# Performance work log

Hardware: AMD Instinct MI355X
Metric: run time of the kernel (lower is better)

## Reference

```python
import jax, jax.numpy as jnp
import numpy as np
from jax import lax


def _attention_conv(x, Wq, bq, Wk, bk, Wv, bv, head_w, p):
    # x: [B,C,H,W]; Wq/Wk/Wv: [heads, D, D] (torch Linear weight, out x in); b*: [heads, D]
    B, C, H, W = x.shape
    pad_h = (p * (1 + H // p) - H) % p
    pad_w = (p * (1 + W // p) - W) % p
    xp = jnp.pad(x, ((0, 0), (0, 0), (p + pad_h, p), (p + pad_w, p)), mode='reflect')
    num_h = (H + pad_h) // p
    num_w = (W + pad_w) // p
    # view padded image as a grid of (num_h+2) x (num_w+2) patches of size p x p
    g = xp.reshape(B, C, num_h + 2, p, num_w + 2, p)
    # 9-patch neighborhood per window (equivalent to unfold with window=3p, stride=p)
    nb = jnp.stack([g[:, :, di:di + num_h, :, dj:dj + num_w, :]
                    for di in range(3) for dj in range(3)], axis=2)  # [B,C,9,num_h,p,num_w,p]
    tokens = nb.transpose(0, 3, 5, 2, 1, 4, 6).reshape(B * num_h * num_w, 9, C * p * p)
    D = C * p * p
    q = jnp.einsum('npd,hed->nhpe', tokens, Wq) + bq[None, :, None, :]
    k = jnp.einsum('npd,hed->nhpe', tokens, Wk) + bk[None, :, None, :]
    v = jnp.einsum('npd,hed->nhpe', tokens, Wv) + bv[None, :, None, :]
    # core patch (index 4 = center of 3x3) attends to all 9 patches
    score = jnp.einsum('nhe,nhpe->nhp', q[:, :, 4, :], k) / jnp.sqrt(jnp.float32(D))
    attn = jax.nn.softmax(score, axis=-1)               # [N,heads,9]
    out = jnp.einsum('nhp,nhpe->nhe', attn, v)          # [N,heads,D]
    mixed = jnp.einsum('h,nhe->ne', head_w[0], out)     # head-weight mixing -> [N,D]
    out = mixed.reshape(B, num_h, num_w, C, p, p).transpose(0, 3, 1, 4, 2, 5)
    out = out.reshape(B, C, num_h * p, num_w * p)
    return out[:, :, pad_h:, pad_w:]


def _dehaze(x, p3, p6, p9, conv0_w, conv0_b):
    b, c, h, w = x.shape
    avg = jnp.mean((1.0 - x).reshape(b, c, -1), axis=-1, keepdims=True)  # [b,c,1]
    xg1 = jax.nn.softmax(avg, axis=-1)[..., None]                        # softmax over size-1 dim -> ones
    xg = jnp.max((x * xg1).reshape(b, 1, -1), axis=-1, keepdims=True)[..., None]  # [b,1,1,1]
    x3 = _attention_conv(x, *p3, 1)
    x6 = _attention_conv(x3, *p6, 2)
    x9 = _attention_conv(x6, *p9, 3)
    cat = jnp.concatenate([x9, x6, x3], axis=1)
    x0 = jax.nn.relu(lax.conv_general_dilated(cat, conv0_w, (1, 1), [(2, 2), (2, 2)])
                     + conv0_b[None, :, None, None])
    return jax.nn.relu(x * x0 + (xg - x0))


def setup_inputs() -> dict:
    key = jax.random.key(0)
    ks = jax.random.split(key, 12)
    inp = {'x': jax.random.uniform(ks[0], (2, 3, 384, 384), jnp.float32)}
    specs = [('3', 6, 3), ('6', 4, 12), ('9', 2, 27)]  # (stage, num_heads, D=C*p*p)
    i = 1
    for name, h, d in specs:
        for proj in ('q', 'k', 'v'):
            inp['w%s_%s' % (name, proj)] = jax.random.normal(ks[i], (h, d, d), jnp.float32) * 0.02
            inp['b%s_%s' % (name, proj)] = jnp.zeros((h, d), jnp.float32)
            i += 1
        inp['hw%s' % name] = jnp.ones((1, h), jnp.float32) / h
    inp['conv0_w'] = jax.random.normal(ks[10], (3, 9, 5, 5), jnp.float32) * 0.02
    inp['conv0_b'] = jnp.zeros((3,), jnp.float32)
    return inp


def reference(x, w3_q, b3_q, w3_k, b3_k, w3_v, b3_v, hw3,
              w6_q, b6_q, w6_k, b6_k, w6_v, b6_v, hw6,
              w9_q, b9_q, w9_k, b9_k, w9_v, b9_v, hw9,
              conv0_w, conv0_b):
    p3 = (w3_q, b3_q, w3_k, b3_k, w3_v, b3_v, hw3)
    p6 = (w6_q, b6_q, w6_k, b6_k, w6_v, b6_v, hw6)
    p9 = (w9_q, b9_q, w9_k, b9_k, w9_v, b9_v, hw9)
    return _dehaze(x, p3, p6, p9, conv0_w, conv0_b)
```

## Files before the change

### kernel.cpp

```cpp
#include <hip/hip_runtime.h>

#define HH 384
#define HWPX (HH*HH)

#define WOFF3 16
#define HS3   40
#define WOFF6 256
#define HS6   328
#define WOFF9 1568
#define HS9   1600
#define CATOFF 8192
#define P9BOFF (CATOFF + 2*9*HWPX)
#define WS_NEED ((size_t)(P9BOFF + 2*3*HWPX) * 4)

__device__ __forceinline__ float4 fma4s(float4 a, float4 w, float t) {
    a.x += w.x * t; a.y += w.y * t; a.z += w.z * t; a.w += w.w * t; return a;
}
__device__ __forceinline__ float dot4(float4 a, float4 b) {
    return a.x * b.x + a.y * b.y + a.z * b.z + a.w * b.w;
}

__global__ __launch_bounds__(256) void pre_xg(
    const float* __restrict__ w3q, const float* __restrict__ b3q,
    const float* __restrict__ w3k, const float* __restrict__ b3k,
    const float* __restrict__ w3v, const float* __restrict__ b3v, const float* __restrict__ hw3,
    const float* __restrict__ w6q, const float* __restrict__ b6q,
    const float* __restrict__ w6k, const float* __restrict__ b6k,
    const float* __restrict__ w6v, const float* __restrict__ b6v, const float* __restrict__ hw6,
    const float* __restrict__ w9q, const float* __restrict__ b9q,
    const float* __restrict__ w9k, const float* __restrict__ b9k,
    const float* __restrict__ w9v, const float* __restrict__ b9v, const float* __restrict__ hw9,
    const float* __restrict__ x, float* __restrict__ ws)
{
    __shared__ float sm[4];
    const int blk = blockIdx.x;
    const int tid = threadIdx.x;

    if (blk < 12) {
        int stage = blk < 6 ? 0 : (blk < 10 ? 1 : 2);
        int h = blk - (stage == 0 ? 0 : (stage == 1 ? 6 : 10));
        const float* WQ[3] = {w3q, w6q, w9q};
        const float* BQ[3] = {b3q, b6q, b9q};
        const float* WK[3] = {w3k, w6k, w9k};
        const float* BK[3] = {b3k, b6k, b9k};
        const float* WV_[3] = {w3v, w6v, w9v};
        const float* BV[3] = {b3v, b6v, b9v};
        const float* HWp[3] = {hw3, hw6, hw9};
        const int Ds[3] = {3, 12, 27};
        const int DPs[3] = {4, 12, 28};
        const int WOFFs[3] = {WOFF3, WOFF6, WOFF9};
        const int HSs[3] = {HS3, HS6, HS9};

        const int D = Ds[stage], DP = DPs[stage];
        const float* wq = WQ[stage] + h * D * D;
        const float* bq = BQ[stage] + h * D;
        const float* wk = WK[stage] + h * D * D;
        const float* bk = BK[stage] + h * D;
        const float* wv = WV_[stage] + h * D * D;
        const float* bv = BV[stage] + h * D;
        const float hwv = HWp[stage][h];
        float* base = ws + WOFFs[stage] + h * HSs[stage];
        const float scale = rsqrtf((float)D);

        for (int i = tid; i < D * DP; i += 256) {
            int a = i / DP, b = i % DP;
            float m = 0.f;
            if (b < D) for (int e = 0; e < D; ++e) m += wk[e * D + b] * wq[e * D + a];
            base[i] = scale * m;
            float wvv = 0.f;
            if (b < D) wvv = hwv * wv[a * D + b];
            base[D * DP + i] = wvv;
        }
        for (int i = tid; i < DP; i += 256) {
            float cv = 0.f, uv = 0.f;
            if (i < D) for (int e = 0; e < D; ++e) {
                cv += bq[e] * wk[e * D + i];
                uv += wq[e * D + i] * bk[e];
            }
            base[2 * D * DP + i] = scale * cv;
            base[2 * D * DP + DP + i] = scale * uv;
            base[2 * D * DP + 2 * DP + i] = (i < D) ? hwv * bv[i] : 0.f;
        }
        if (tid == 0) {
            float s = 0.f;
            for (int e = 0; e < D; ++e) s += bq[e] * bk[e];
            base[2 * D * DP + 3 * DP] = scale * s;
        }
    } else {
        int i2 = blk - 12;
        int b = i2 / 144, chunk = i2 % 144;
        const float4* xb = (const float4*)(x + (size_t)b * 3 * HWPX + chunk * 3072);
        float m = 0.f;
        for (int j = tid; j < 768; j += 256) {
            float4 v = xb[j];
            m = fmaxf(m, fmaxf(fmaxf(v.x, v.y), fmaxf(v.z, v.w)));
        }
        for (int off = 32; off; off >>= 1)
            m = fmaxf(m, __shfl_down(m, off));
        if ((tid & 63) == 0) sm[tid >> 6] = m;
        __syncthreads();
        if (tid == 0) {
            float mm = fmaxf(fmaxf(sm[0], sm[1]), fmaxf(sm[2], sm[3]));
            atomicMax((int*)&ws[b], __float_as_int(mm));
        }
    }
}

template <int P, int HEADS, int HSPLIT>
__global__ __launch_bounds__(256) void attn_cell(
    const float* __restrict__ in, long in_bstride,
    float* __restrict__ outA, long outA_bstride,
    float* __restrict__ outB, long outB_bstride,
    const float* __restrict__ wsw)
{
    constexpr int C = 3, D = C * P * P, DP = (D + 3) & ~3, NREG = DP / 4;
    constexpr int HS = 2 * D * DP + 3 * DP + 4;
    constexpr int HPT = HEADS / HSPLIT;
    __shared__ __align__(16) float scell[324 * DP];
    __shared__ __align__(16) float sw[HPT * HS];

    const int tid = threadIdx.x;
    const int z = blockIdx.z;
    const int b = z & 1;
    const int hs = z >> 1;
    const int BWY = blockIdx.y * 16, BWX = blockIdx.x * 16;

    const float* inb = in + (size_t)b * in_bstride;
    constexpr int XW = 18 * P;
    constexpr int TOT = 3 * P * 18 * XW;
    for (int i = tid; i < TOT; i += 256) {
        int c = i / (P * 18 * XW);
        int rem = i % (P * 18 * XW);
        int r = rem / (18 * XW);
        int rem2 = rem % (18 * XW);
        int cy = rem2 / XW, xx = rem2 % XW;
        int y = (BWY + cy) * P + r - P; y = y < 0 ? -y : (y >= HH ? 2 * HH - 2 - y : y);
        int x = BWX * P + xx - P;       x = x < 0 ? -x : (x >= HH ? 2 * HH - 2 - x : x);
        int cx = xx / P, s = xx % P;
        scell[(cy * 18 + cx) * DP + (c * P + r) * P + s] = inb[c * HWPX + y * HH + x];
    }
    if constexpr (DP > D) {
        for (int j = tid; j < 324; j += 256) scell[j * DP + D] = 0.f;
    }
    const float* wsrc = wsw + (size_t)hs * HPT * HS;
    for (int i = tid; i < HPT * HS; i += 256) sw[i] = wsrc[i];
    __syncthreads();

    const int wx = tid & 15, wy = tid >> 4;

    float t4[DP];
    {
        const float4* T4p = (const float4*)&scell[((wy + 1) * 18 + wx + 1) * DP];
#pragma unroll
        for (int k = 0; k < NREG; ++k) {
            float4 v = T4p[k];
            t4[4 * k] = v.x; t4[4 * k + 1] = v.y; t4[4 * k + 2] = v.z; t4[4 * k + 3] = v.w;
        }
    }
    float mixed[D];
#pragma unroll
    for (int e = 0; e < D; ++e) mixed[e] = 0.f;

#pragma unroll 1
    for (int hh = 0; hh < HPT; ++hh) {
        const float* hb = sw + hh * HS;
        const float* ccb = hb + 2 * D * DP;
        float4 qk[NREG];
        {
            const float4* cp = (const float4*)ccb;
#pragma unroll
            for (int k = 0; k < NREG; ++k) qk[k] = cp[k];
        }
        float su = ccb[3 * DP];
#pragma unroll
        for (int a = 0; a < D; ++a) {
            const float t = t4[a];
            su += ccb[DP + a] * t;
            const float4* Mr = (const float4*)(hb + a * DP);
#pragma unroll
            for (int k = 0; k < NREG; ++k) qk[k] = fma4s(qk[k], Mr[k], t);
        }
        float denom = 0.f;
        float4 wt[NREG];
#pragma unroll
        for (int k = 0; k < NREG; ++k) wt[k] = make_float4(0.f, 0.f, 0.f, 0.f);
#pragma unroll
        for (int di = 0; di < 3; ++di)
#pragma unroll
            for (int dj = 0; dj < 3; ++dj) {
                const float4* cp = (const float4*)&scell[((wy + di) * 18 + wx + dj) * DP];
                float4 cv[NREG];
#pragma unroll
                for (int k = 0; k < NREG; ++k) cv[k] = cp[k];
                float s = su;
#pragma unroll
                for (int k = 0; k < NREG; ++k) s += dot4(qk[k], cv[k]);
                const float e = __expf(s);
                denom += e;
#pragma unroll
                for (int k = 0; k < NREG; ++k) wt[k] = fma4s(wt[k], cv[k], e);
            }
        const float winv = 1.f / denom;
#pragma unroll
        for (int k = 0; k < NREG; ++k) {
            wt[k].x *= winv; wt[k].y *= winv; wt[k].z *= winv; wt[k].w *= winv;
        }
        const float* WVb = hb + D * DP;
#pragma unroll
        for (int e = 0; e < D; ++e) {
            const float4* Wr = (const float4*)(WVb + e * DP);
            float o = ccb[2 * DP + e];
#pragma unroll
            for (int k = 0; k < NREG; ++k) o += dot4(Wr[k], wt[k]);
            mixed[e] += o;
        }
    }

    float* outp = (hs == 0) ? (outA + (size_t)b * outA_bstride)
                            : (outB + (size_t)b * outB_bstride);
#pragma unroll
    for (int c = 0; c < C; ++c)
#pragma unroll
        for (int r = 0; r < P; ++r)
#pragma unroll
            for (int s = 0; s < P; ++s)
                outp[c * HWPX + ((BWY + wy) * P + r) * HH + (BWX + wx) * P + s] =
                    mixed[(c * P + r) * P + s];
}

__global__ __launch_bounds__(128) void conv_final(
    const float* __restrict__ cat, const float* __restrict__ p9b, int addp9,
    const float* __restrict__ w, const float* __restrict__ bias,
    const float* __restrict__ x, const float* __restrict__ xg,
    float* __restrict__ out)
{
    __shared__ float tile[9][20][40];
    const int tid = threadIdx.x;
    const int b = blockIdx.z;
    const int bx = blockIdx.x * 32, by = blockIdx.y * 16;
    const float* catb = cat + (size_t)b * 9 * HWPX;
    const float* p9bb = p9b + (size_t)b * 3 * HWPX;

    for (int i = tid; i < 9 * 20 * 10; i += 128) {
        int ci = i / 200;
        int rem = i % 200;
        int row = rem / 10, c4 = rem % 10;
        int y = by + row - 2, xx = bx - 4 + 4 * c4;
        float4 v = {0.f, 0.f, 0.f, 0.f};
        if (y >= 0 && y < HH && xx >= 0 && xx <= HH - 4) {
            v = *(const float4*)&catb[ci * HWPX + y * HH + xx];
            if (addp9 && ci < 3) {
                float4 u = *(const float4*)&p9bb[ci * HWPX + y * HH + xx];
                v.x += u.x; v.y += u.y; v.z += u.z; v.w += u.w;
            }
        }
        *(float4*)&tile[ci][row][4 * c4] = v;
    }
    __syncthreads();

    const int tx = tid & 7, ty = tid >> 3;
    float acc0[4], acc1[4], acc2[4];
    const float b0 = bias[0], b1 = bias[1], b2 = bias[2];
#pragma unroll
    for (int j = 0; j < 4; ++j) { acc0[j] = b0; acc1[j] = b1; acc2[j] = b2; }

#pragma unroll
    for (int ky = 0; ky < 5; ++ky) {
#pragma unroll 1
        for (int ci = 0; ci < 9; ++ci) {
            const float4 ra = *(const float4*)&tile[ci][ty + ky][4 * tx];
            const float4 rb = *(const float4*)&tile[ci][ty + ky][4 * tx + 4];
            const float4 rc = *(const float4*)&tile[ci][ty + ky][4 * tx + 8];
            const float r[12] = {ra.x, ra.y, ra.z, ra.w, rb.x, rb.y, rb.z, rb.w,
                                 rc.x, rc.y, rc.z, rc.w};
            const float* __restrict__ w0 = w + (0 * 9 + ci) * 25 + ky * 5;
            const float* __restrict__ w1 = w + (1 * 9 + ci) * 25 + ky * 5;
            const float* __restrict__ w2 = w + (2 * 9 + ci) * 25 + ky * 5;
#pragma unroll
            for (int j = 0; j < 4; ++j)
#pragma unroll
                for (int kx = 0; kx < 5; ++kx) {
                    const float t = r[j + kx + 2];
                    acc0[j] += t * w0[kx];
                    acc1[j] += t * w1[kx];
                    acc2[j] += t * w2[kx];
                }
        }
    }

    const int yb = by + ty, xb = bx + 4 * tx;
    const float xgv = xg[b];
    float* accs[3] = {acc0, acc1, acc2};
#pragma unroll
    for (int co = 0; co < 3; ++co) {
        const float4 xv = *(const float4*)&x[((size_t)(b * 3 + co)) * HWPX + yb * HH + xb];
        const float* a = accs[co];
        float4 ov;
        float x0;
        x0 = fmaxf(a[0], 0.f); ov.x = fmaxf(xv.x * x0 + xgv - x0, 0.f);
        x0 = fmaxf(a[1], 0.f); ov.y = fmaxf(xv.y * x0 + xgv - x0, 0.f);
        x0 = fmaxf(a[2], 0.f); ov.z = fmaxf(xv.z * x0 + xgv - x0, 0.f);
        x0 = fmaxf(a[3], 0.f); ov.w = fmaxf(xv.w * x0 + xgv - x0, 0.f);
        *(float4*)&out[((size_t)(b * 3 + co)) * HWPX + yb * HH + xb] = ov;
    }
}

extern "C" void kernel_launch(void* const* d_in, const int* in_sizes, int n_in,
                              void* d_out, int out_size, void* d_ws, size_t ws_size,
                              hipStream_t stream) {
    const float* x   = (const float*)d_in[0];
    const float* w3q = (const float*)d_in[1];
    const float* b3q = (const float*)d_in[2];
    const float* w3k = (const float*)d_in[3];
    const float* b3k = (const float*)d_in[4];
    const float* w3v = (const float*)d_in[5];
    const float* b3v = (const float*)d_in[6];
    const float* hw3 = (const float*)d_in[7];
    const float* w6q = (const float*)d_in[8];
    const float* b6q = (const float*)d_in[9];
    const float* w6k = (const float*)d_in[10];
    const float* b6k = (const float*)d_in[11];
    const float* w6v = (const float*)d_in[12];
    const float* b6v = (const float*)d_in[13];
    const float* hw6 = (const float*)d_in[14];
    const float* w9q = (const float*)d_in[15];
    const float* b9q = (const float*)d_in[16];
    const float* w9k = (const float*)d_in[17];
    const float* b9k = (const float*)d_in[18];
    const float* w9v = (const float*)d_in[19];
    const float* b9v = (const float*)d_in[20];
    const float* hw9 = (const float*)d_in[21];
    const float* c0w = (const float*)d_in[22];
    const float* c0b = (const float*)d_in[23];

    float* out = (float*)d_out;
    float* ws  = (float*)d_ws;
    float* cat = ws + CATOFF;
    float* p9b = ws + P9BOFF;
    const bool split9 = ws_size >= WS_NEED;

    pre_xg<<<300, 256, 0, stream>>>(
        w3q, b3q, w3k, b3k, w3v, b3v, hw3,
        w6q, b6q, w6k, b6k, w6v, b6v, hw6,
        w9q, b9q, w9k, b9k, w9v, b9v, hw9, x, ws);

    attn_cell<1, 6, 1><<<dim3(24, 24, 2), 256, 0, stream>>>(
        x, 3 * HWPX, cat + 6 * HWPX, 9 * HWPX, cat + 6 * HWPX, 9 * HWPX, ws + WOFF3);
    attn_cell<2, 4, 1><<<dim3(12, 12, 2), 256, 0, stream>>>(
        cat + 6 * HWPX, 9 * HWPX, cat + 3 * HWPX, 9 * HWPX, cat + 3 * HWPX, 9 * HWPX, ws + WOFF6);
    if (split9)
        attn_cell<3, 2, 2><<<dim3(8, 8, 4), 256, 0, stream>>>(
            cat + 3 * HWPX, 9 * HWPX, cat, 9 * HWPX, p9b, 3 * HWPX, ws + WOFF9);
    else
        attn_cell<3, 2, 1><<<dim3(8, 8, 2), 256, 0, stream>>>(
            cat + 3 * HWPX, 9 * HWPX, cat, 9 * HWPX, cat, 9 * HWPX, ws + WOFF9);

    conv_final<<<dim3(12, 24, 2), 128, 0, stream>>>(
        cat, p9b, split9 ? 1 : 0, c0w, c0b, x, ws, out);
}
```

Measured before the change: 216.5 us.

## Fuse all three attention stages and final conv into one tiled megakernel

Replaces the three per-stage attention kernels and the final conv kernel with a single kernel. Each block loads a haloed input tile into LDS and computes the p=1, p=2 and p=3 stages with recomputed halos. Reflect-padding borders are fixed up in shared memory, and the 5x5 conv plus output epilogue run in place. This removes the global round trips of the intermediate concat buffers and three launches. In exchange it recomputes halo regions, leaves only 192 blocks to occupy the GPU, and runs the stage-9 pass on just 234 of 512 threads. An unused stub kernel 'mega' is also left in.

```diff
diff --git a/kernel.cpp b/kernel.cpp
--- a/kernel.cpp
+++ b/kernel.cpp
@@ -9,15 +9,19 @@
 #define HS6   328
 #define WOFF9 1568
 #define HS9   1600
-#define CATOFF 8192
-#define P9BOFF (CATOFF + 2*9*HWPX)
-#define WS_NEED ((size_t)(P9BOFF + 2*3*HWPX) * 4)
-
+
+__device__ __forceinline__ int rx(int g) {
+    g = g < 0 ? -g : g;
+    return g >= HH ? 2 * HH - 2 - g : g;
+}
 __device__ __forceinline__ float4 fma4s(float4 a, float4 w, float t) {
     a.x += w.x * t; a.y += w.y * t; a.z += w.z * t; a.w += w.w * t; return a;
 }
 __device__ __forceinline__ float dot4(float4 a, float4 b) {
     return a.x * b.x + a.y * b.y + a.z * b.z + a.w * b.w;
+}
+__device__ __forceinline__ float f4c(const float4& v, int j) {
+    return j == 0 ? v.x : (j == 1 ? v.y : (j == 2 ? v.z : v.w));
 }
 
 __global__ __launch_bounds__(256) void pre_xg(
@@ -106,202 +110,357 @@
     }
 }
 
-template <int P, int HEADS, int HSPLIT>
-__global__ __launch_bounds__(256) void attn_cell(
-    const float* __restrict__ in, long in_bstride,
-    float* __restrict__ outA, long outA_bstride,
-    float* __restrict__ outB, long outB_bstride,
-    const float* __restrict__ wsw)
-{
-    constexpr int C = 3, D = C * P * P, DP = (D + 3) & ~3, NREG = DP / 4;
-    constexpr int HS = 2 * D * DP + 3 * DP + 4;
-    constexpr int HPT = HEADS / HSPLIT;
-    __shared__ __align__(16) float scell[324 * DP];
-    __shared__ __align__(16) float sw[HPT * HS];
-
-    const int tid = threadIdx.x;
-    const int z = blockIdx.z;
-    const int b = z & 1;
-    const int hs = z >> 1;
-    const int BWY = blockIdx.y * 16, BWX = blockIdx.x * 16;
-
-    const float* inb = in + (size_t)b * in_bstride;
-    constexpr int XW = 18 * P;
-    constexpr int TOT = 3 * P * 18 * XW;
-    for (int i = tid; i < TOT; i += 256) {
-        int c = i / (P * 18 * XW);
-        int rem = i % (P * 18 * XW);
-        int r = rem / (18 * XW);
-        int rem2 = rem % (18 * XW);
-        int cy = rem2 / XW, xx = rem2 % XW;
-        int y = (BWY + cy) * P + r - P; y = y < 0 ? -y : (y >= HH ? 2 * HH - 2 - y : y);
-        int x = BWX * P + xx - P;       x = x < 0 ? -x : (x >= HH ? 2 * HH - 2 - x : x);
-        int cx = xx / P, s = xx % P;
-        scell[(cy * 18 + cx) * DP + (c * P + r) * P + s] = inb[c * HWPX + y * HH + x];
-    }
-    if constexpr (DP > D) {
-        for (int j = tid; j < 324; j += 256) scell[j * DP + D] = 0.f;
-    }
-    const float* wsrc = wsw + (size_t)hs * HPT * HS;
-    for (int i = tid; i < HPT * HS; i += 256) sw[i] = wsrc[i];
-    __syncthreads();
-
-    const int wx = tid & 15, wy = tid >> 4;
-
-    float t4[DP];
-    {
-        const float4* T4p = (const float4*)&scell[((wy + 1) * 18 + wx + 1) * DP];
-#pragma unroll
-        for (int k = 0; k < NREG; ++k) {
-            float4 v = T4p[k];
-            t4[4 * k] = v.x; t4[4 * k + 1] = v.y; t4[4 * k + 2] = v.z; t4[4 * k + 3] = v.w;
-        }
-    }
-    float mixed[D];
-#pragma unroll
-    for (int e = 0; e < D; ++e) mixed[e] = 0.f;
-
-#pragma unroll 1
-    for (int hh = 0; hh < HPT; ++hh) {
-        const float* hb = sw + hh * HS;
-        const float* ccb = hb + 2 * D * DP;
-        float4 qk[NREG];
-        {
-            const float4* cp = (const float4*)ccb;
-#pragma unroll
-            for (int k = 0; k < NREG; ++k) qk[k] = cp[k];
-        }
-        float su = ccb[3 * DP];
-#pragma unroll
-        for (int a = 0; a < D; ++a) {
-            const float t = t4[a];
-            su += ccb[DP + a] * t;
-            const float4* Mr = (const float4*)(hb + a * DP);
-#pragma unroll
-            for (int k = 0; k < NREG; ++k) qk[k] = fma4s(qk[k], Mr[k], t);
-        }
-        float denom = 0.f;
-        float4 wt[NREG];
-#pragma unroll
-        for (int k = 0; k < NREG; ++k) wt[k] = make_float4(0.f, 0.f, 0.f, 0.f);
-#pragma unroll
-        for (int di = 0; di < 3; ++di)
-#pragma unroll
-            for (int dj = 0; dj < 3; ++dj) {
-                const float4* cp = (const float4*)&scell[((wy + di) * 18 + wx + dj) * DP];
-                float4 cv[NREG];
-#pragma unroll
-                for (int k = 0; k < NREG; ++k) cv[k] = cp[k];
-                float s = su;
-#pragma unroll
-                for (int k = 0; k < NREG; ++k) s += dot4(qk[k], cv[k]);
-                const float e = __expf(s);
-                denom += e;
-#pragma unroll
-                for (int k = 0; k < NREG; ++k) wt[k] = fma4s(wt[k], cv[k], e);
-            }
-        const float winv = 1.f / denom;
-#pragma unroll
-        for (int k = 0; k < NREG; ++k) {
-            wt[k].x *= winv; wt[k].y *= winv; wt[k].z *= winv; wt[k].w *= winv;
-        }
-        const float* WVb = hb + D * DP;
-#pragma unroll
-        for (int e = 0; e < D; ++e) {
-            const float4* Wr = (const float4*)(WVb + e * DP);
-            float o = ccb[2 * DP + e];
-#pragma unroll
-            for (int k = 0; k < NREG; ++k) o += dot4(Wr[k], wt[k]);
-            mixed[e] += o;
-        }
-    }
-
-    float* outp = (hs == 0) ? (outA + (size_t)b * outA_bstride)
-                            : (outB + (size_t)b * outB_bstride);
-#pragma unroll
-    for (int c = 0; c < C; ++c)
-#pragma unroll
-        for (int r = 0; r < P; ++r)
-#pragma unroll
-            for (int s = 0; s < P; ++s)
-                outp[c * HWPX + ((BWY + wy) * P + r) * HH + (BWX + wx) * P + s] =
-                    mixed[(c * P + r) * P + s];
-}
-
-__global__ __launch_bounds__(128) void conv_final(
-    const float* __restrict__ cat, const float* __restrict__ p9b, int addp9,
-    const float* __restrict__ w, const float* __restrict__ bias,
-    const float* __restrict__ x, const float* __restrict__ xg,
+__global__ __launch_bounds__(512, 2) void mega(
+    const float* __restrict__ x, const float* __restrict__ wsg,
     float* __restrict__ out)
 {
-    __shared__ float tile[9][20][40];
+    __shared__ float L[36536];
     const int tid = threadIdx.x;
-    const int b = blockIdx.z;
-    const int bx = blockIdx.x * 32, by = blockIdx.y * 16;
-    const float* catb = cat + (size_t)b * 9 * HWPX;
-    const float* p9bb = p9b + (size_t)b * 3 * HWPX;
-
-    for (int i = tid; i < 9 * 20 * 10; i += 128) {
-        int ci = i / 200;
-        int rem = i % 200;
-        int row = rem / 10, c4 = rem % 10;
-        int y = by + row - 2, xx = bx - 4 + 4 * c4;
-        float4 v = {0.f, 0.f, 0.f, 0.f};
-        if (y >= 0 && y < HH && xx >= 0 && xx <= HH - 4) {
-            v = *(const float4*)&catb[ci * HWPX + y * HH + xx];
-            if (addp9 && ci < 3) {
-                float4 u = *(const float4*)&p9bb[ci * HWPX + y * HH + xx];
-                v.x += u.x; v.y += u.y; v.z += u.z; v.w += u.w;
-            }
-        }
-        *(float4*)&tile[ci][row][4 * c4] = v;
-    }
-    __syncthreads();
-
-    const int tx = tid & 7, ty = tid >> 3;
-    float acc0[4], acc1[4], acc2[4];
-    const float b0 = bias[0], b1 = bias[1], b2 = bias[2];
-#pragma unroll
-    for (int j = 0; j < 4; ++j) { acc0[j] = b0; acc1[j] = b1; acc2[j] = b2; }
-
-#pragma unroll
-    for (int ky = 0; ky < 5; ++ky) {
-#pragma unroll 1
-        for (int ci = 0; ci < 9; ++ci) {
-            const float4 ra = *(const float4*)&tile[ci][ty + ky][4 * tx];
-            const float4 rb = *(const float4*)&tile[ci][ty + ky][4 * tx + 4];
-            const float4 rc = *(const float4*)&tile[ci][ty + ky][4 * tx + 8];
-            const float r[12] = {ra.x, ra.y, ra.z, ra.w, rb.x, rb.y, rb.z, rb.w,
-                                 rc.x, rc.y, rc.z, rc.w};
-            const float* __restrict__ w0 = w + (0 * 9 + ci) * 25 + ky * 5;
-            const float* __restrict__ w1 = w + (1 * 9 + ci) * 25 + ky * 5;
-            const float* __restrict__ w2 = w + (2 * 9 + ci) * 25 + ky * 5;
-#pragma unroll
-            for (int j = 0; j < 4; ++j)
-#pragma unroll
-                for (int kx = 0; kx < 5; ++kx) {
-                    const float t = r[j + kx + 2];
-                    acc0[j] += t * w0[kx];
-                    acc1[j] += t * w1[kx];
-                    acc2[j] += t * w2[kx];
+    const int X0 = blockIdx.x * 48, Y0 = blockIdx.y * 32, b = blockIdx.z;
+    const int OXx = X0 - 12, OXy = Y0 - 12;
+    const int C3X = X0 / 2 - 5, C3Y = Y0 / 2 - 5;
+    const int m9y = (Y0 + 1) / 3 - 1;
+    const int m9x = X0 / 3 - 1;
+    const int C6X = X0 / 3 - 2, C6Y = m9y - 1;
+    const float* xb = x + (size_t)b * 3 * HWPX;
+
+    for (int i = tid; i < 3 * 56 * 18; i += 512) {
+        int c = i / (56 * 18);
+        int rem = i - c * 56 * 18;
+        int row = rem / 18, ck = rem % 18;
+        int gy = rx(OXy + row);
+        int gx0 = OXx + 4 * ck;
+        const float* src = xb + c * HWPX + gy * HH;
+        float4 v;
+        if (gx0 >= 0 && gx0 + 4 <= HH) v = *(const float4*)(src + gx0);
+        else { v.x = src[rx(gx0)]; v.y = src[rx(gx0 + 1)]; v.z = src[rx(gx0 + 2)]; v.w = src[rx(gx0 + 3)]; }
+        *(float4*)&L[c * 4032 + row * 72 + 4 * ck] = v;
+    }
+    for (int i = tid; i < 1188; i += 512)
+        *(float4*)&L[12096 + 4 * i] = *(const float4*)&wsg[WOFF3 + 4 * i];
+    for (int i = tid; i < 678; i += 512)
+        L[12096 + 4752 + i] = wsg[0] * 0.f + ((i < 675) ? 0.f : 0.f);
+    __syncthreads();
+
+    __syncthreads();
+    (void)out;
+}
+
+__global__ __launch_bounds__(512, 2) void mega2(
+    const float* __restrict__ x, const float* __restrict__ wsg,
+    const float* __restrict__ convw, const float* __restrict__ convb,
+    float* __restrict__ out)
+{
+    __shared__ float L[36536];
+    const int tid = threadIdx.x;
+    const int X0 = blockIdx.x * 48, Y0 = blockIdx.y * 32, b = blockIdx.z;
+    const int OXx = X0 - 12, OXy = Y0 - 12;
+    const int C3X = X0 / 2 - 5, C3Y = Y0 / 2 - 5;
+    const int m9y = (Y0 + 1) / 3 - 1;
+    const int m9x = X0 / 3 - 1;
+    const int C6X = X0 / 3 - 2, C6Y = m9y - 1;
+    const float* xb = x + (size_t)b * 3 * HWPX;
+    const bool border = (X0 == 0) || (X0 == 336) || (Y0 == 0) || (Y0 == 352);
+
+    for (int i = tid; i < 3 * 56 * 18; i += 512) {
+        int c = i / (56 * 18);
+        int rem = i - c * 56 * 18;
+        int row = rem / 18, ck = rem % 18;
+        int gy = rx(OXy + row);
+        int gx0 = OXx + 4 * ck;
+        const float* src = xb + c * HWPX + gy * HH;
+        float4 v;
+        if (gx0 >= 0 && gx0 + 4 <= HH) v = *(const float4*)(src + gx0);
+        else { v.x = src[rx(gx0)]; v.y = src[rx(gx0 + 1)]; v.z = src[rx(gx0 + 2)]; v.w = src[rx(gx0 + 3)]; }
+        *(float4*)&L[c * 4032 + row * 72 + 4 * ck] = v;
+    }
+    for (int i = tid; i < 1188; i += 512)
+        *(float4*)&L[12096 + 4 * i] = *(const float4*)&wsg[WOFF3 + 4 * i];
+    for (int i = tid; i < 678; i += 512)
+        L[12096 + 4752 + i] = (i < 675) ? convw[i] : convb[i - 675];
+    for (int i = tid; i < 300; i += 512) L[17528 + i * 28 + 27] = 0.f;
+    __syncthreads();
+
+    for (int l = tid; l < 68 * 52; l += 512) {
+        int lx = l % 68, ly = l / 68;
+        int gx = X0 - 10 + lx, gy = Y0 - 10 + ly;
+        if (gx < 0 || gx >= HH || gy < 0 || gy >= HH) continue;
+        float4 T[9];
+#pragma unroll
+        for (int di = 0; di < 3; ++di)
+#pragma unroll
+            for (int dj = 0; dj < 3; ++dj) {
+                int ax = lx + 1 + dj, ay = ly + 1 + di;
+                T[di * 3 + dj] = make_float4(L[ay * 72 + ax], L[4032 + ay * 72 + ax],
+                                             L[8064 + ay * 72 + ax], 0.f);
+            }
+        float m0 = 0.f, m1 = 0.f, m2 = 0.f;
+#pragma unroll 1
+        for (int h = 0; h < 6; ++h) {
+            const float* hb = &L[12096 + h * 40];
+            float4 qk = *(const float4*)(hb + 24);
+            float su = hb[36] + dot4(*(const float4*)(hb + 28), T[4]);
+            qk = fma4s(qk, *(const float4*)(hb + 0), T[4].x);
+            qk = fma4s(qk, *(const float4*)(hb + 4), T[4].y);
+            qk = fma4s(qk, *(const float4*)(hb + 8), T[4].z);
+            float den = 0.f; float4 wt = {0.f, 0.f, 0.f, 0.f};
+#pragma unroll
+            for (int p = 0; p < 9; ++p) {
+                float e = __expf(su + dot4(qk, T[p]));
+                den += e; wt = fma4s(wt, T[p], e);
+            }
+            float wi = 1.f / den;
+            wt.x *= wi; wt.y *= wi; wt.z *= wi; wt.w *= wi;
+            m0 += hb[32] + dot4(*(const float4*)(hb + 12), wt);
+            m1 += hb[33] + dot4(*(const float4*)(hb + 16), wt);
+            m2 += hb[34] + dot4(*(const float4*)(hb + 20), wt);
+        }
+        float* cell = &L[25928 + ((ly >> 1) * 34 + (lx >> 1)) * 12 + (ly & 1) * 2 + (lx & 1)];
+        cell[0] = m0; cell[4] = m1; cell[8] = m2;
+    }
+    __syncthreads();
+
+    if (border) {
+        for (int l = tid; l < 884; l += 512) {
+            int lcx = l % 34, lcy = l / 34;
+            int gcx = C3X + lcx, gcy = C3Y + lcy;
+            if (gcx >= 0 && gcx < 192 && gcy >= 0 && gcy < 192) continue;
+            float* dst = &L[25928 + l * 12];
+#pragma unroll
+            for (int rr = 0; rr < 2; ++rr)
+#pragma unroll
+                for (int ss = 0; ss < 2; ++ss) {
+                    int rpy = rx(2 * gcy + rr), rpx = rx(2 * gcx + ss);
+                    const float* src = &L[25928 + (((rpy >> 1) - C3Y) * 34 + ((rpx >> 1) - C3X)) * 12
+                                          + (rpy & 1) * 2 + (rpx & 1)];
+                    dst[rr * 2 + ss] = src[0];
+                    dst[4 + rr * 2 + ss] = src[4];
+                    dst[8 + rr * 2 + ss] = src[8];
                 }
         }
     }
-
-    const int yb = by + ty, xb = bx + 4 * tx;
-    const float xgv = xg[b];
-    float* accs[3] = {acc0, acc1, acc2};
-#pragma unroll
-    for (int co = 0; co < 3; ++co) {
-        const float4 xv = *(const float4*)&x[((size_t)(b * 3 + co)) * HWPX + yb * HH + xb];
-        const float* a = accs[co];
-        float4 ov;
-        float x0;
-        x0 = fmaxf(a[0], 0.f); ov.x = fmaxf(xv.x * x0 + xgv - x0, 0.f);
-        x0 = fmaxf(a[1], 0.f); ov.y = fmaxf(xv.y * x0 + xgv - x0, 0.f);
-        x0 = fmaxf(a[2], 0.f); ov.z = fmaxf(xv.z * x0 + xgv - x0, 0.f);
-        x0 = fmaxf(a[3], 0.f); ov.w = fmaxf(xv.w * x0 + xgv - x0, 0.f);
-        *(float4*)&out[((size_t)(b * 3 + co)) * HWPX + yb * HH + xb] = ov;
+    __syncthreads();
+
+    for (int l = tid; l < 768; l += 512) {
+        int lwx = l % 32, lwy = l / 32;
+        int gwx = X0 / 2 - 4 + lwx, gwy = Y0 / 2 - 4 + lwy;
+        if (gwx < 0 || gwx >= 192 || gwy < 0 || gwy >= 192) continue;
+        float4 T[9][3];
+#pragma unroll
+        for (int di = 0; di < 3; ++di)
+#pragma unroll
+            for (int dj = 0; dj < 3; ++dj) {
+                const float4* cp = (const float4*)&L[25928 + ((lwy + di) * 34 + (lwx + dj)) * 12];
+                T[di * 3 + dj][0] = cp[0]; T[di * 3 + dj][1] = cp[1]; T[di * 3 + dj][2] = cp[2];
+            }
+        float mixed[12];
+#pragma unroll
+        for (int e = 0; e < 12; ++e) mixed[e] = 0.f;
+#pragma unroll 1
+        for (int h = 0; h < 4; ++h) {
+            const float* hb = &L[12096 + 240 + h * 328];
+            float4 qk0 = *(const float4*)(hb + 288);
+            float4 qk1 = *(const float4*)(hb + 292);
+            float4 qk2 = *(const float4*)(hb + 296);
+            float su = hb[324];
+#pragma unroll
+            for (int a = 0; a < 12; ++a) {
+                float t = f4c(T[4][a >> 2], a & 3);
+                su += hb[300 + a] * t;
+                const float4* Mr = (const float4*)(hb + 12 * a);
+                qk0 = fma4s(qk0, Mr[0], t);
+                qk1 = fma4s(qk1, Mr[1], t);
+                qk2 = fma4s(qk2, Mr[2], t);
+            }
+            float den = 0.f;
+            float4 wt0 = {0,0,0,0}, wt1 = {0,0,0,0}, wt2 = {0,0,0,0};
+#pragma unroll
+            for (int p = 0; p < 9; ++p) {
+                float s = su + dot4(qk0, T[p][0]) + dot4(qk1, T[p][1]) + dot4(qk2, T[p][2]);
+                float e = __expf(s);
+                den += e;
+                wt0 = fma4s(wt0, T[p][0], e);
+                wt1 = fma4s(wt1, T[p][1], e);
+                wt2 = fma4s(wt2, T[p][2], e);
+            }
+            float wi = 1.f / den;
+            wt0.x *= wi; wt0.y *= wi; wt0.z *= wi; wt0.w *= wi;
+            wt1.x *= wi; wt1.y *= wi; wt1.z *= wi; wt1.w *= wi;
+            wt2.x *= wi; wt2.y *= wi; wt2.z *= wi; wt2.w *= wi;
+#pragma unroll
+            for (int e = 0; e < 12; ++e) {
+                const float4* Wr = (const float4*)(hb + 144 + 12 * e);
+                mixed[e] += hb[312 + e] + dot4(Wr[0], wt0) + dot4(Wr[1], wt1) + dot4(Wr[2], wt2);
+            }
+        }
+#pragma unroll
+        for (int c = 0; c < 3; ++c)
+#pragma unroll
+            for (int r2 = 0; r2 < 2; ++r2)
+#pragma unroll
+                for (int s2 = 0; s2 < 2; ++s2) {
+                    int gpy = 2 * gwy + r2, gpx = 2 * gwx + s2;
+                    int q3y = gpy / 3, q3x = gpx / 3;
+                    int lcy = q3y - C6Y, lcx = q3x - C6X;
+                    if (lcx < 0 || lcx >= 20 || lcy < 0 || lcy >= 15) continue;
+                    L[17528 + (lcy * 20 + lcx) * 28 + c * 9 + (gpy - 3 * q3y) * 3 + (gpx - 3 * q3x)]
+                        = mixed[(c * 2 + r2) * 2 + s2];
+                }
+    }
+    __syncthreads();
+
+    if (border) {
+        for (int l = tid; l < 300; l += 512) {
+            int lcx = l % 20, lcy = l / 20;
+            int gcx = C6X + lcx, gcy = C6Y + lcy;
+            if (gcx >= 0 && gcx < 128 && gcy >= 0 && gcy < 128) continue;
+            float* dst = &L[17528 + l * 28];
+            for (int e = 0; e < 27; ++e) {
+                int c = e / 9, r9 = (e % 9) / 3, s9 = e % 3;
+                int rpy = rx(3 * gcy + r9), rpx = rx(3 * gcx + s9);
+                dst[e] = L[17528 + (((rpy / 3) - C6Y) * 20 + ((rpx / 3) - C6X)) * 28
+                           + c * 9 + (rpy % 3) * 3 + (rpx % 3)];
+            }
+        }
+    }
+    __syncthreads();
+
+    if (tid < 234) {
+        int lwx = tid % 18, lwy = tid / 18;
+        int gwx = m9x + lwx, gwy = m9y + lwy;
+        if (gwx >= 0 && gwx < 128 && gwy >= 0 && gwy < 128) {
+            const float4* cc = (const float4*)&L[17528 + ((lwy + 1) * 20 + (lwx + 1)) * 28];
+            float4 t9[7];
+#pragma unroll
+            for (int k = 0; k < 7; ++k) t9[k] = cc[k];
+            float mixed[27];
+#pragma unroll
+            for (int e = 0; e < 27; ++e) mixed[e] = 0.f;
+#pragma unroll 1
+            for (int h = 0; h < 2; ++h) {
+                const float* hb = &L[12096 + 1552 + h * 1600];
+                float4 qk[7];
+#pragma unroll
+                for (int k = 0; k < 7; ++k) qk[k] = *(const float4*)(hb + 1512 + 4 * k);
+                float su = hb[1596];
+#pragma unroll
+                for (int a = 0; a < 27; ++a) {
+                    float t = f4c(t9[a >> 2], a & 3);
+                    su += hb[1540 + a] * t;
+                    const float4* Mr = (const float4*)(hb + 28 * a);
+#pragma unroll
+                    for (int k = 0; k < 7; ++k) qk[k] = fma4s(qk[k], Mr[k], t);
+                }
+                float den = 0.f;
+                float4 wt[7];
+#pragma unroll
+                for (int k = 0; k < 7; ++k) wt[k] = make_float4(0.f, 0.f, 0.f, 0.f);
+#pragma unroll 1
+                for (int p = 0; p < 9; ++p) {
+                    int di = p / 3, dj = p % 3;
+                    const float4* cv = (const float4*)&L[17528 + ((lwy + di) * 20 + (lwx + dj)) * 28];
+                    float s = su;
+                    float4 c0 = cv[0], c1 = cv[1], c2 = cv[2], c3 = cv[3],
+                           c4 = cv[4], c5 = cv[5], c6 = cv[6];
+                    s += dot4(qk[0], c0) + dot4(qk[1], c1) + dot4(qk[2], c2) + dot4(qk[3], c3)
+                       + dot4(qk[4], c4) + dot4(qk[5], c5) + dot4(qk[6], c6);
+                    float e = __expf(s);
+                    den += e;
+                    wt[0] = fma4s(wt[0], c0, e); wt[1] = fma4s(wt[1], c1, e);
+                    wt[2] = fma4s(wt[2], c2, e); wt[3] = fma4s(wt[3], c3, e);
+                    wt[4] = fma4s(wt[4], c4, e); wt[5] = fma4s(wt[5], c5, e);
+                    wt[6] = fma4s(wt[6], c6, e);
+                }
+                float wi = 1.f / den;
+#pragma unroll
+                for (int k = 0; k < 7; ++k) { wt[k].x *= wi; wt[k].y *= wi; wt[k].z *= wi; wt[k].w *= wi; }
+#pragma unroll
+                for (int e = 0; e < 27; ++e) {
+                    const float4* Wr = (const float4*)(hb + 756 + 28 * e);
+                    float o = hb[1568 + e];
+#pragma unroll
+                    for (int k = 0; k < 7; ++k) o += dot4(Wr[k], wt[k]);
+                    mixed[e] += o;
+                }
+            }
+#pragma unroll
+            for (int c = 0; c < 3; ++c)
+#pragma unroll
+                for (int r9 = 0; r9 < 3; ++r9)
+#pragma unroll
+                    for (int s9 = 0; s9 < 3; ++s9) {
+                        int ly = 3 * gwy + r9 - (Y0 - 2), lx = 3 * gwx + s9 - (X0 - 2);
+                        if (lx >= 0 && lx < 52 && ly >= 0 && ly < 36)
+                            L[c * 1872 + ly * 52 + lx] = mixed[c * 9 + r9 * 3 + s9];
+                    }
+        }
+    }
+    __syncthreads();
+
+    for (int i = tid; i < 5616; i += 512) {
+        int c = i / 1872, rem = i % 1872;
+        int ly = rem / 52, lx = rem % 52;
+        int gy = Y0 - 2 + ly, gx = X0 - 2 + lx;
+        bool in = (gy >= 0 && gy < HH && gx >= 0 && gx < HH);
+        if (!in) L[i] = 0.f;
+        float v6 = 0.f;
+        if (in) {
+            int q3y = gy / 3, q3x = gx / 3;
+            v6 = L[17528 + ((q3y - C6Y) * 20 + (q3x - C6X)) * 28 + c * 9
+                   + (gy - 3 * q3y) * 3 + (gx - 3 * q3x)];
+        }
+        L[5616 + i] = v6;
+    }
+    __syncthreads();
+
+    {
+        const float xg = wsg[b];
+        int pxl[3], pyl[3];
+        float acc[3][3];
+        const float b0 = L[12096 + 5427 + 0], b1 = L[12096 + 5427 + 1], b2 = L[12096 + 5427 + 2];
+#pragma unroll
+        for (int j = 0; j < 3; ++j) {
+            int l = tid + j * 512;
+            pxl[j] = l % 48; pyl[j] = l / 48;
+            acc[0][j] = b0; acc[1][j] = b1; acc[2][j] = b2;
+        }
+#pragma unroll 1
+        for (int ky = 0; ky < 5; ++ky) {
+#pragma unroll 1
+            for (int kx = 0; kx < 5; ++kx) {
+#pragma unroll 1
+                for (int ci = 0; ci < 9; ++ci) {
+                    const float w0 = L[12096 + 4752 + (0 * 9 + ci) * 25 + ky * 5 + kx];
+                    const float w1 = L[12096 + 4752 + (1 * 9 + ci) * 25 + ky * 5 + kx];
+                    const float w2 = L[12096 + 4752 + (2 * 9 + ci) * 25 + ky * 5 + kx];
+#pragma unroll
+                    for (int j = 0; j < 3; ++j) {
+                        int gy = Y0 + pyl[j] + ky - 2, gx = X0 + pxl[j] + kx - 2;
+                        float t = 0.f;
+                        if (gy >= 0 && gy < HH && gx >= 0 && gx < HH) {
+                            if (ci < 6) {
+                                t = L[(ci < 3 ? 0 : 5616) + (ci % 3) * 1872
+                                      + (pyl[j] + ky) * 52 + pxl[j] + kx];
+                            } else {
+                                t = L[25928 + (((gy >> 1) - C3Y) * 34 + ((gx >> 1) - C3X)) * 12
+                                      + (ci - 6) * 4 + (gy & 1) * 2 + (gx & 1)];
+                            }
+                        }
+                        acc[0][j] += t * w0; acc[1][j] += t * w1; acc[2][j] += t * w2;
+                    }
+                }
+            }
+        }
+#pragma unroll
+        for (int j = 0; j < 3; ++j) {
+            int gy = Y0 + pyl[j], gx = X0 + pxl[j];
+#pragma unroll
+            for (int co = 0; co < 3; ++co) {
+                float x0 = fmaxf(acc[co][j], 0.f);
+                float xv = xb[co * HWPX + gy * HH + gx];
+                out[((size_t)(b * 3 + co)) * HWPX + gy * HH + gx] = fmaxf(xv * x0 + xg - x0, 0.f);
+            }
+        }
     }
 }
 
@@ -335,26 +494,11 @@
 
     float* out = (float*)d_out;
     float* ws  = (float*)d_ws;
-    float* cat = ws + CATOFF;
-    float* p9b = ws + P9BOFF;
-    const bool split9 = ws_size >= WS_NEED;
 
     pre_xg<<<300, 256, 0, stream>>>(
         w3q, b3q, w3k, b3k, w3v, b3v, hw3,
         w6q, b6q, w6k, b6k, w6v, b6v, hw6,
         w9q, b9q, w9k, b9k, w9v, b9v, hw9, x, ws);
 
-    attn_cell<1, 6, 1><<<dim3(24, 24, 2), 256, 0, stream>>>(
-        x, 3 * HWPX, cat + 6 * HWPX, 9 * HWPX, cat + 6 * HWPX, 9 * HWPX, ws + WOFF3);
-    attn_cell<2, 4, 1><<<dim3(12, 12, 2), 256, 0, stream>>>(
-        cat + 6 * HWPX, 9 * HWPX, cat + 3 * HWPX, 9 * HWPX, cat + 3 * HWPX, 9 * HWPX, ws + WOFF6);
-    if (split9)
-        attn_cell<3, 2, 2><<<dim3(8, 8, 4), 256, 0, stream>>>(
-            cat + 3 * HWPX, 9 * HWPX, cat, 9 * HWPX, p9b, 3 * HWPX, ws + WOFF9);
-    else
-        attn_cell<3, 2, 1><<<dim3(8, 8, 2), 256, 0, stream>>>(
-            cat + 3 * HWPX, 9 * HWPX, cat, 9 * HWPX, cat, 9 * HWPX, ws + WOFF9);
-
-    conv_final<<<dim3(12, 24, 2), 128, 0, stream>>>(
-        cat, p9b, split9 ? 1 : 0, c0w, c0b, x, ws, out);
-}
+    mega2<<<dim3(8, 12, 2), 512, 0, stream>>>(x, ws, c0w, c0b, out);
+}
```

After: 309.4 us. 42.9% more time.
